# Optimization experiments

Hardware: AMD Instinct MI355X
Metric: run time of the kernel (lower is better)

The kernel has to match this reference:

```python
import jax, jax.numpy as jnp
import numpy as np

DISTANCE_WEIGHT = 1.001  # self.distence_weight in the torch module


def setup_inputs() -> dict:
    key = jax.random.key(0)
    k1, k2 = jax.random.split(key)
    B, DIM_IN, DIM_OUT = 1024, 512, 512
    x = jax.random.normal(k1, (B, DIM_IN), dtype=jnp.float32)
    centers = jax.random.normal(k2, (DIM_OUT, DIM_IN), dtype=jnp.float32)
    beta = jnp.ones((DIM_OUT,), dtype=jnp.float32)
    return {"x": x, "centers": centers, "beta": beta}


def reference(x, centers, beta):
    # L1 pairwise distance: [B, dim_out]
    sim = jnp.sum(jnp.abs(x[:, None, :] - centers[None, :, :]), axis=-1)
    # negate, shift by global max * distance_weight, scale by beta
    sim = -sim + jnp.max(sim) * DISTANCE_WEIGHT
    return beta * sim
```

## Files before the change

### kernel.cpp

```cpp
#include <hip/hip_runtime.h>


typedef _Float16 h2 __attribute__((ext_vector_type(2)));
typedef float f4 __attribute__((ext_vector_type(4)));
typedef unsigned int u32x4 __attribute__((ext_vector_type(4)));
typedef unsigned int u32x2 __attribute__((ext_vector_type(2)));

#define DIM_O 512
#define DIM_K 512
#define BM 16
#define BN 32
#define BK 64
#define LSTRIDE 36
#define W_DIST 1.001f

__device__ __forceinline__ h2 as_h2(unsigned int u){ h2 r; __builtin_memcpy(&r,&u,4); return r; }
__device__ __forceinline__ unsigned int as_u(h2 h){ unsigned int r; __builtin_memcpy(&r,&h,4); return r; }
__device__ __forceinline__ unsigned int cvt2(float a, float b){
    auto h = __builtin_amdgcn_cvt_pkrtz(a, b);
    unsigned int r; __builtin_memcpy(&r, &h, 4); return r;
}

__global__ __launch_bounds__(64) void k_sim(const float* __restrict__ X,
                                            const float* __restrict__ C,
                                            float* __restrict__ S,
                                            float* __restrict__ bmax)
{
    __shared__ __align__(16) h2 xs[BM][LSTRIDE];
    __shared__ __align__(16) h2 cs[BN][LSTRIDE];
    const int tid = threadIdx.x;
    const int bx = blockIdx.x & 15;
    const int by = blockIdx.x >> 4;
    const int row0 = by * BM, col0 = bx * BN;
    const int tr = tid >> 4;
    const int tc = tid & 15;
    float acc[4][2] = {};
    const h2 one2 = {(_Float16)1.f, (_Float16)1.f};

    f4 xv[4], cv[8];
    const int srow = tid >> 4, skv = tid & 15;
#pragma unroll
    for (int p = 0; p < 4; ++p)
        xv[p] = *(const f4*)(X + (row0 + srow + 4 * p) * DIM_K + 4 * skv);
#pragma unroll
    for (int p = 0; p < 8; ++p)
        cv[p] = *(const f4*)(C + (col0 + srow + 4 * p) * DIM_K + 4 * skv);

    for (int t = 0; t < 8; ++t) {
        __syncthreads();
#pragma unroll
        for (int p = 0; p < 4; ++p) {
            u32x2 w; w[0] = cvt2(xv[p].x, xv[p].y); w[1] = cvt2(xv[p].z, xv[p].w);
            *(u32x2*)&xs[srow + 4 * p][skv * 2] = w;
        }
#pragma unroll
        for (int p = 0; p < 8; ++p) {
            u32x2 w; w[0] = cvt2(cv[p].x, cv[p].y); w[1] = cvt2(cv[p].z, cv[p].w);
            *(u32x2*)&cs[srow + 4 * p][skv * 2] = w;
        }
        __syncthreads();

        const int kn = (t < 7) ? (t + 1) * BK : 0;
#pragma unroll
        for (int p = 0; p < 4; ++p)
            xv[p] = *(const f4*)(X + (row0 + srow + 4 * p) * DIM_K + kn + 4 * skv);
#pragma unroll
        for (int p = 0; p < 8; ++p)
            cv[p] = *(const f4*)(C + (col0 + srow + 4 * p) * DIM_K + kn + 4 * skv);

#pragma unroll
        for (int g = 0; g < 8; ++g) {
            u32x4 xr[4], cr[2];
#pragma unroll
            for (int i = 0; i < 4; ++i)
                xr[i] = *(const u32x4*)&xs[tr * 4 + i][g * 4];
            cr[0] = *(const u32x4*)&cs[tc][g * 4];
            cr[1] = *(const u32x4*)&cs[tc + 16][g * 4];
#pragma unroll
            for (int k2 = 0; k2 < 4; ++k2) {
#pragma unroll
                for (int i = 0; i < 4; ++i) {
                    h2 a = as_h2(xr[i][k2]);
#pragma unroll
                    for (int j = 0; j < 2; ++j) {
                        h2 d = a - as_h2(cr[j][k2]);
                        h2 ad = as_h2(as_u(d) & 0x7fff7fffu);
                        acc[i][j] = __builtin_amdgcn_fdot2(ad, one2, acc[i][j], false);
                    }
                }
            }
        }
    }

    float m = 0.f;
#pragma unroll
    for (int i = 0; i < 4; ++i) {
        const int r = row0 + tr * 4 + i;
        S[r * DIM_O + col0 + tc]      = acc[i][0];
        S[r * DIM_O + col0 + tc + 16] = acc[i][1];
        m = fmaxf(m, fmaxf(acc[i][0], acc[i][1]));
    }
#pragma unroll
    for (int off = 32; off > 0; off >>= 1)
        m = fmaxf(m, __shfl_xor(m, off, 64));
    if (tid == 0) bmax[blockIdx.x] = m;
}

__global__ __launch_bounds__(256) void k_out(float* __restrict__ S,
                                             const float* __restrict__ beta,
                                             const float* __restrict__ bmax)
{
    const int tid = threadIdx.x;
    const int lane = tid & 63;
    float m = 0.f;
#pragma unroll
    for (int i = 0; i < 16; ++i)
        m = fmaxf(m, bmax[lane + 64 * i]);
#pragma unroll
    for (int off = 32; off > 0; off >>= 1)
        m = fmaxf(m, __shfl_xor(m, off, 64));
    const float shift = m * W_DIST;

    const int f = blockIdx.x * 256 + tid;
    f4 s = ((const f4*)S)[f];
    f4 b = ((const f4*)beta)[f & 127];
    f4 r;
    r.x = b.x * (shift - s.x);
    r.y = b.y * (shift - s.y);
    r.z = b.z * (shift - s.z);
    r.w = b.w * (shift - s.w);
    ((f4*)S)[f] = r;
}

extern "C" void kernel_launch(void* const* d_in, const int* in_sizes, int n_in,
                              void* d_out, int out_size, void* d_ws, size_t ws_size,
                              hipStream_t stream) {
    const float* X = (const float*)d_in[0];
    const float* C = (const float*)d_in[1];
    const float* beta = (const float*)d_in[2];
    float* S = (float*)d_out;
    float* bmax = (float*)d_ws;
    k_sim<<<1024, 64, 0, stream>>>(X, C, S, bmax);
    k_out<<<512, 256, 0, stream>>>(S, beta, bmax);
}
```

Measured before the change: 81.18 us.

## Pre-convert inputs to fp16 and stream tiles into LDS with triple buffering

Adds a separate conversion kernel that writes X and centers as fp16 into workspace. The similarity kernel then loads those fp16 tiles straight into LDS with global_load_lds and a three-stage buffer managed by vmcnt waits, replacing the register-staged loads, in-kernel conversion and block syncs. This halves the bytes read by the main kernel and overlaps loads with compute. In exchange it adds a third launch and a workspace round trip, and it drops the __syncthreads calls, relying on a single-wave block for LDS ordering.

```diff
diff --git a/kernel.cpp b/kernel.cpp
--- a/kernel.cpp
+++ b/kernel.cpp
@@ -3,79 +3,98 @@
 
 typedef _Float16 h2 __attribute__((ext_vector_type(2)));
 typedef float f4 __attribute__((ext_vector_type(4)));
+typedef unsigned int u32;
 typedef unsigned int u32x4 __attribute__((ext_vector_type(4)));
 typedef unsigned int u32x2 __attribute__((ext_vector_type(2)));
+typedef unsigned short u16;
 
 #define DIM_O 512
 #define DIM_K 512
-#define BM 16
-#define BN 32
-#define BK 64
-#define LSTRIDE 36
 #define W_DIST 1.001f
 
-__device__ __forceinline__ h2 as_h2(unsigned int u){ h2 r; __builtin_memcpy(&r,&u,4); return r; }
-__device__ __forceinline__ unsigned int as_u(h2 h){ unsigned int r; __builtin_memcpy(&r,&h,4); return r; }
-__device__ __forceinline__ unsigned int cvt2(float a, float b){
+__device__ __forceinline__ h2 as_h2(u32 u){ h2 r; __builtin_memcpy(&r,&u,4); return r; }
+__device__ __forceinline__ u32 as_u(h2 h){ u32 r; __builtin_memcpy(&r,&h,4); return r; }
+__device__ __forceinline__ u32 cvt2(float a, float b){
     auto h = __builtin_amdgcn_cvt_pkrtz(a, b);
-    unsigned int r; __builtin_memcpy(&r, &h, 4); return r;
+    u32 r; __builtin_memcpy(&r, &h, 4); return r;
 }
 
-__global__ __launch_bounds__(64) void k_sim(const float* __restrict__ X,
-                                            const float* __restrict__ C,
+__device__ __forceinline__ void gload16(const void* g, void* l) {
+    __builtin_amdgcn_global_load_lds(
+        (const __attribute__((address_space(1))) u32*)g,
+        (__attribute__((address_space(3))) u32*)l, 16, 0, 0);
+}
+
+__global__ __launch_bounds__(256) void k_cvt(const float* __restrict__ X,
+                                             const float* __restrict__ C,
+                                             u32x2* __restrict__ Xh,
+                                             u32x2* __restrict__ Ch)
+{
+    const int f = blockIdx.x * 256 + threadIdx.x;
+    const int NX = (1024 * DIM_K) / 4;
+    f4 v;
+    if (f < NX) v = *(const f4*)(X + 4 * f);
+    else        v = *(const f4*)(C + 4 * (f - NX));
+    u32x2 w; w[0] = cvt2(v.x, v.y); w[1] = cvt2(v.z, v.w);
+    if (f < NX) Xh[f] = w; else Ch[f - NX] = w;
+}
+
+__global__ __launch_bounds__(64) void k_sim(const u16* __restrict__ Xh,
+                                            const u16* __restrict__ Ch,
                                             float* __restrict__ S,
                                             float* __restrict__ bmax)
 {
-    __shared__ __align__(16) h2 xs[BM][LSTRIDE];
-    __shared__ __align__(16) h2 cs[BN][LSTRIDE];
+    __shared__ __align__(16) char lds[3 * 6144];
     const int tid = threadIdx.x;
     const int bx = blockIdx.x & 15;
     const int by = blockIdx.x >> 4;
-    const int row0 = by * BM, col0 = bx * BN;
+    const int row0 = by * 16, col0 = bx * 32;
     const int tr = tid >> 4;
     const int tc = tid & 15;
+
+    const char* xsrc = (const char*)(Xh + (row0 + (tid & 15)) * DIM_K + (tid >> 4) * 8);
+    const char* csrc = (const char*)(Ch + (col0 + (tid & 31)) * DIM_K + (tid >> 5) * 8);
+
+    char* b0 = lds;
+    char* b1 = lds + 6144;
+    char* b2 = lds + 12288;
+
+    auto stage = [&](int q, char* p) {
+        const char* xq = xsrc + q * 128;
+        const char* cq = csrc + q * 128;
+        gload16(xq,      p);
+        gload16(xq + 64, p + 1024);
+        gload16(cq,      p + 2048);
+        gload16(cq + 32, p + 3072);
+        gload16(cq + 64, p + 4096);
+        gload16(cq + 96, p + 5120);
+    };
+
     float acc[4][2] = {};
     const h2 one2 = {(_Float16)1.f, (_Float16)1.f};
 
-    f4 xv[4], cv[8];
-    const int srow = tid >> 4, skv = tid & 15;
-#pragma unroll
-    for (int p = 0; p < 4; ++p)
-        xv[p] = *(const f4*)(X + (row0 + srow + 4 * p) * DIM_K + 4 * skv);
-#pragma unroll
-    for (int p = 0; p < 8; ++p)
-        cv[p] = *(const f4*)(C + (col0 + srow + 4 * p) * DIM_K + 4 * skv);
+    stage(0, b0);
+    stage(1, b1);
 
     for (int t = 0; t < 8; ++t) {
-        __syncthreads();
-#pragma unroll
-        for (int p = 0; p < 4; ++p) {
-            u32x2 w; w[0] = cvt2(xv[p].x, xv[p].y); w[1] = cvt2(xv[p].z, xv[p].w);
-            *(u32x2*)&xs[srow + 4 * p][skv * 2] = w;
-        }
-#pragma unroll
-        for (int p = 0; p < 8; ++p) {
-            u32x2 w; w[0] = cvt2(cv[p].x, cv[p].y); w[1] = cvt2(cv[p].z, cv[p].w);
-            *(u32x2*)&cs[srow + 4 * p][skv * 2] = w;
-        }
-        __syncthreads();
+        if (t < 7) { asm volatile("s_waitcnt vmcnt(6)" ::: "memory"); }
+        else       { asm volatile("s_waitcnt vmcnt(0)" ::: "memory"); }
+        __builtin_amdgcn_sched_barrier(0);
+        if (t < 6) stage(t + 2, b2);
 
-        const int kn = (t < 7) ? (t + 1) * BK : 0;
-#pragma unroll
-        for (int p = 0; p < 4; ++p)
-            xv[p] = *(const f4*)(X + (row0 + srow + 4 * p) * DIM_K + kn + 4 * skv);
-#pragma unroll
-        for (int p = 0; p < 8; ++p)
-            cv[p] = *(const f4*)(C + (col0 + srow + 4 * p) * DIM_K + kn + 4 * skv);
-
+        const char* xb = b0;
+        const char* cb = b0 + 2048;
 #pragma unroll
         for (int g = 0; g < 8; ++g) {
-            u32x4 xr[4], cr[2];
-#pragma unroll
-            for (int i = 0; i < 4; ++i)
-                xr[i] = *(const u32x4*)&xs[tr * 4 + i][g * 4];
-            cr[0] = *(const u32x4*)&cs[tc][g * 4];
-            cr[1] = *(const u32x4*)&cs[tc + 16][g * 4];
+            const int xo = (g >> 2) * 1024 + (g & 3) * 256 + tr * 64;
+            const int co = (g >> 1) * 1024 + (g & 1) * 512 + tc * 16;
+            u32x4 xr[4]; u32x4 cr[2];
+            xr[0] = *(const u32x4*)(xb + xo);
+            xr[1] = *(const u32x4*)(xb + xo + 16);
+            xr[2] = *(const u32x4*)(xb + xo + 32);
+            xr[3] = *(const u32x4*)(xb + xo + 48);
+            cr[0] = *(const u32x4*)(cb + co);
+            cr[1] = *(const u32x4*)(cb + co + 256);
 #pragma unroll
             for (int k2 = 0; k2 < 4; ++k2) {
 #pragma unroll
@@ -90,6 +109,7 @@
                 }
             }
         }
+        char* tmp = b0; b0 = b1; b1 = b2; b2 = tmp;
     }
 
     float m = 0.f;
@@ -140,6 +160,9 @@
     const float* beta = (const float*)d_in[2];
     float* S = (float*)d_out;
     float* bmax = (float*)d_ws;
-    k_sim<<<1024, 64, 0, stream>>>(X, C, S, bmax);
+    u16* Xh = (u16*)((char*)d_ws + 4096);
+    u16* Ch = (u16*)((char*)d_ws + 4096 + 1024 * 1024);
+    k_cvt<<<768, 256, 0, stream>>>(X, C, (u32x2*)Xh, (u32x2*)Ch);
+    k_sim<<<1024, 64, 0, stream>>>(Xh, Ch, S, bmax);
     k_out<<<512, 256, 0, stream>>>(S, beta, bmax);
 }
```

Result: no change. 81.83 us (+0.8%).

## Repack LDS tiles into a contiguous fragment layout and drop block barriers

Applied to the files above, without the earlier changes.

The padded 2D shared-memory arrays are replaced by a flat buffer. Each thread now stores a 16-byte packed fp16 fragment at a thread-indexed offset, and the compute loop reads fragments at offsets matching that layout. This gives wider LDS stores and reads that should be free of bank conflicts. The global loads are remapped so each thread fetches 8 consecutive floats per row segment. Both __syncthreads calls are removed, which relies on the block being a single 64-lane wavefront and on the compiler keeping LDS accesses in order. That assumption is fragile if the compiler reorders the accesses.

```diff
diff --git a/kernel.cpp b/kernel.cpp
--- a/kernel.cpp
+++ b/kernel.cpp
@@ -3,22 +3,18 @@
 
 typedef _Float16 h2 __attribute__((ext_vector_type(2)));
 typedef float f4 __attribute__((ext_vector_type(4)));
+typedef unsigned int u32;
 typedef unsigned int u32x4 __attribute__((ext_vector_type(4)));
-typedef unsigned int u32x2 __attribute__((ext_vector_type(2)));
 
 #define DIM_O 512
 #define DIM_K 512
-#define BM 16
-#define BN 32
-#define BK 64
-#define LSTRIDE 36
 #define W_DIST 1.001f
 
-__device__ __forceinline__ h2 as_h2(unsigned int u){ h2 r; __builtin_memcpy(&r,&u,4); return r; }
-__device__ __forceinline__ unsigned int as_u(h2 h){ unsigned int r; __builtin_memcpy(&r,&h,4); return r; }
-__device__ __forceinline__ unsigned int cvt2(float a, float b){
+__device__ __forceinline__ h2 as_h2(u32 u){ h2 r; __builtin_memcpy(&r,&u,4); return r; }
+__device__ __forceinline__ u32 as_u(h2 h){ u32 r; __builtin_memcpy(&r,&h,4); return r; }
+__device__ __forceinline__ u32 cvt2(float a, float b){
     auto h = __builtin_amdgcn_cvt_pkrtz(a, b);
-    unsigned int r; __builtin_memcpy(&r, &h, 4); return r;
+    u32 r; __builtin_memcpy(&r, &h, 4); return r;
 }
 
 __global__ __launch_bounds__(64) void k_sim(const float* __restrict__ X,
@@ -26,56 +22,72 @@
                                             float* __restrict__ S,
                                             float* __restrict__ bmax)
 {
-    __shared__ __align__(16) h2 xs[BM][LSTRIDE];
-    __shared__ __align__(16) h2 cs[BN][LSTRIDE];
+    __shared__ __align__(16) char lds[6144];
     const int tid = threadIdx.x;
     const int bx = blockIdx.x & 15;
     const int by = blockIdx.x >> 4;
-    const int row0 = by * BM, col0 = bx * BN;
+    const int row0 = by * 16, col0 = bx * 32;
     const int tr = tid >> 4;
     const int tc = tid & 15;
+
+    const float* xsrc = X + (row0 + (tid & 15)) * DIM_K + (tid >> 4) * 8;
+    const float* csrc = C + (col0 + (tid & 31)) * DIM_K + (tid >> 5) * 8;
+    char* xdst = lds + tid * 16;
+    char* cdst = lds + 2048 + tid * 16;
+
+    f4 xv[4], cv[8];
+    auto loadc = [&](int t) {
+        const float* xq = xsrc + t * 64;
+        const float* cq = csrc + t * 64;
+#pragma unroll
+        for (int i = 0; i < 2; ++i)
+#pragma unroll
+            for (int h = 0; h < 2; ++h)
+                xv[2 * i + h] = *(const f4*)(xq + i * 32 + h * 4);
+#pragma unroll
+        for (int i = 0; i < 4; ++i)
+#pragma unroll
+            for (int h = 0; h < 2; ++h)
+                cv[2 * i + h] = *(const f4*)(cq + i * 16 + h * 4);
+    };
+
     float acc[4][2] = {};
     const h2 one2 = {(_Float16)1.f, (_Float16)1.f};
 
-    f4 xv[4], cv[8];
-    const int srow = tid >> 4, skv = tid & 15;
-#pragma unroll
-    for (int p = 0; p < 4; ++p)
-        xv[p] = *(const f4*)(X + (row0 + srow + 4 * p) * DIM_K + 4 * skv);
-#pragma unroll
-    for (int p = 0; p < 8; ++p)
-        cv[p] = *(const f4*)(C + (col0 + srow + 4 * p) * DIM_K + 4 * skv);
+    loadc(0);
 
     for (int t = 0; t < 8; ++t) {
-        __syncthreads();
 #pragma unroll
-        for (int p = 0; p < 4; ++p) {
-            u32x2 w; w[0] = cvt2(xv[p].x, xv[p].y); w[1] = cvt2(xv[p].z, xv[p].w);
-            *(u32x2*)&xs[srow + 4 * p][skv * 2] = w;
+        for (int i = 0; i < 2; ++i) {
+            u32x4 w;
+            w[0] = cvt2(xv[2 * i].x,     xv[2 * i].y);
+            w[1] = cvt2(xv[2 * i].z,     xv[2 * i].w);
+            w[2] = cvt2(xv[2 * i + 1].x, xv[2 * i + 1].y);
+            w[3] = cvt2(xv[2 * i + 1].z, xv[2 * i + 1].w);
+            *(u32x4*)(xdst + i * 1024) = w;
         }
 #pragma unroll
-        for (int p = 0; p < 8; ++p) {
-            u32x2 w; w[0] = cvt2(cv[p].x, cv[p].y); w[1] = cvt2(cv[p].z, cv[p].w);
-            *(u32x2*)&cs[srow + 4 * p][skv * 2] = w;
+        for (int i = 0; i < 4; ++i) {
+            u32x4 w;
+            w[0] = cvt2(cv[2 * i].x,     cv[2 * i].y);
+            w[1] = cvt2(cv[2 * i].z,     cv[2 * i].w);
+            w[2] = cvt2(cv[2 * i + 1].x, cv[2 * i + 1].y);
+            w[3] = cvt2(cv[2 * i + 1].z, cv[2 * i + 1].w);
+            *(u32x4*)(cdst + i * 1024) = w;
         }
-        __syncthreads();
-
-        const int kn = (t < 7) ? (t + 1) * BK : 0;
-#pragma unroll
-        for (int p = 0; p < 4; ++p)
-            xv[p] = *(const f4*)(X + (row0 + srow + 4 * p) * DIM_K + kn + 4 * skv);
-#pragma unroll
-        for (int p = 0; p < 8; ++p)
-            cv[p] = *(const f4*)(C + (col0 + srow + 4 * p) * DIM_K + kn + 4 * skv);
+        if (t < 7) loadc(t + 1);
 
 #pragma unroll
         for (int g = 0; g < 8; ++g) {
+            const int xo = (g >> 2) * 1024 + (g & 3) * 256 + tr * 64;
+            const int co = 2048 + (g >> 1) * 1024 + (g & 1) * 512 + tc * 16;
             u32x4 xr[4], cr[2];
-#pragma unroll
-            for (int i = 0; i < 4; ++i)
-                xr[i] = *(const u32x4*)&xs[tr * 4 + i][g * 4];
-            cr[0] = *(const u32x4*)&cs[tc][g * 4];
-            cr[1] = *(const u32x4*)&cs[tc + 16][g * 4];
+            xr[0] = *(const u32x4*)(lds + xo);
+            xr[1] = *(const u32x4*)(lds + xo + 16);
+            xr[2] = *(const u32x4*)(lds + xo + 32);
+            xr[3] = *(const u32x4*)(lds + xo + 48);
+            cr[0] = *(const u32x4*)(lds + co);
+            cr[1] = *(const u32x4*)(lds + co + 256);
 #pragma unroll
             for (int k2 = 0; k2 < 4; ++k2) {
 #pragma unroll
```

After: 80.40 us (median of 2 runs). No clear change (-1.0%).
